# Kernel optimization log

Measured on AMD Instinct MI355X. Metric: run time of the kernel, lower is better.

## Reference

```python
import jax, jax.numpy as jnp
import numpy as np

B, L, W = 4096, 30, 5          # batch, MAX_TOKEN_LENGTH, WINDOW_SIZE
A, E = 30, 128                 # ALPHABET_SIZE, embedding dim
C = 40                         # OUT_CHANNELS
H, T = 128, 3                  # LSTM_UNITS, num CRF tags
LIN = W * C                    # 200
EPS = 1e-5


def setup_inputs():
    key = jax.random.key(0)
    ks = jax.random.split(key, 24)
    def rn(k, shape, s=0.1):
        return jax.random.normal(k, shape, jnp.float32) * s
    return {
        'x': jax.random.randint(ks[0], (B, L, W), 0, A, jnp.int32),
        'emb': rn(ks[1], (A, E), 1.0),
        'conv_w': rn(ks[2], (C, E, 3)),
        'conv_b': rn(ks[3], (C,)),
        'bn1_g': 1.0 + rn(ks[4], (C,)),
        'bn1_b': rn(ks[5], (C,)),
        'bn1_m': rn(ks[6], (C,)),
        'bn1_v': 0.5 + jax.random.uniform(ks[7], (C,), jnp.float32),
        'w_ih_f': rn(ks[8], (4 * H, LIN)),
        'w_hh_f': rn(ks[9], (4 * H, H)),
        'b_f': rn(ks[10], (4 * H,)),
        'w_ih_b': rn(ks[11], (4 * H, LIN)),
        'w_hh_b': rn(ks[12], (4 * H, H)),
        'b_b': rn(ks[13], (4 * H,)),
        'bn2_g': 1.0 + rn(ks[14], (2 * H,)),
        'bn2_b': rn(ks[15], (2 * H,)),
        'bn2_m': rn(ks[16], (2 * H,)),
        'bn2_v': 0.5 + jax.random.uniform(ks[17], (2 * H,), jnp.float32),
        'fc_w': rn(ks[18], (T, 2 * H)),
        'fc_b': rn(ks[19], (T,)),
        'trans': rn(ks[20], (T, T)),
        'start_t': rn(ks[21], (T,)),
        'end_t': rn(ks[22], (T,)),
    }


def _lstm_dir(seq, w_ih, w_hh, b, reverse):
    # seq: [B, L, F]; torch gate order i, f, g, o
    xs = jnp.einsum('blf,gf->lbg', seq, w_ih) + b  # [L, B, 4H]
    h0 = jnp.zeros((seq.shape[0], H), seq.dtype)
    def step(carry, xt):
        h, c = carry
        z = xt + h @ w_hh.T
        i, f, g, o = jnp.split(z, 4, axis=-1)
        c = jax.nn.sigmoid(f) * c + jax.nn.sigmoid(i) * jnp.tanh(g)
        h = jax.nn.sigmoid(o) * jnp.tanh(c)
        return (h, c), h
    _, hs = jax.lax.scan(step, (h0, h0), xs, reverse=reverse)
    return hs.transpose(1, 0, 2)  # [B, L, H]


def _viterbi(emis, mask, trans, start_t, end_t):
    # emis: [B, L, T], mask: [B, L] bool
    score = start_t + emis[:, 0]                      # [B, T]
    def step(score, inp):
        e_t, m_t = inp                                # [B, T], [B]
        cand = score[:, :, None] + trans              # [B, Tprev, Tnext]
        ptr = jnp.argmax(cand, axis=1)                # [B, T]
        new = jnp.max(cand, axis=1) + e_t
        return jnp.where(m_t[:, None], new, score), ptr
    score, hist = jax.lax.scan(
        step, score, (emis[:, 1:].transpose(1, 0, 2), mask[:, 1:].T))
    score = score + end_t
    best = jnp.max(score, axis=1)                     # [B] path scores
    last = jnp.argmax(score, axis=1)                  # [B]
    def back(tag, inp):
        h_t, m_t = inp
        prev = jnp.take_along_axis(h_t, tag[:, None], axis=1)[:, 0]
        tag = jnp.where(m_t, prev, tag)
        return tag, tag
    _, ys = jax.lax.scan(back, last, (hist, mask[:, 1:].T), reverse=True)
    tags = jnp.concatenate([ys, last[None]], axis=0).T  # [B, L]
    return best, tags


def reference(x, emb, conv_w, conv_b, bn1_g, bn1_b, bn1_m, bn1_v,
              w_ih_f, w_hh_f, b_f, w_ih_b, w_hh_b, b_b,
              bn2_g, bn2_b, bn2_m, bn2_v, fc_w, fc_b, trans, start_t, end_t):
    mask = x[:, :, 2] > 0                             # [B, L]
    e = emb[x.reshape(B * L, W)]                      # [N, W, E]  (dropout=eval noop)
    e = e.transpose(0, 2, 1)                          # [N, E, W]
    y = jax.lax.conv_general_dilated(
        e, conv_w, (1,), [(1, 1)],
        dimension_numbers=('NCH', 'OIH', 'NCH')) + conv_b[:, None]
    # BatchNorm1d (inference, running stats)
    y = (y - bn1_m[:, None]) * (bn1_g / jnp.sqrt(bn1_v + EPS))[:, None] + bn1_b[:, None]
    y = jax.nn.relu(y)
    # MaxPool1d(k=3, stride=1, pad=1): length preserved
    y = jax.lax.reduce_window(y, -jnp.inf, jax.lax.max,
                              (1, 1, 3), (1, 1, 1),
                              [(0, 0), (0, 0), (1, 1)])
    y = y.reshape(B, L, LIN)                          # torch.flatten is channel-major = row-major reshape
    hf = _lstm_dir(y, w_ih_f, w_hh_f, b_f, False)
    hb = _lstm_dir(y, w_ih_b, w_hh_b, b_b, True)
    h = jnp.concatenate([hf, hb], axis=-1)            # [B, L, 2H]
    h = (h - bn2_m) * (bn2_g / jnp.sqrt(bn2_v + EPS)) + bn2_b
    emis = h @ fc_w.T + fc_b                          # [B, L, T]
    return _viterbi(emis, mask, trans, start_t, end_t)
```

## Files before the change

kernel.cpp:

```cpp
#include <hip/hip_runtime.h>
#include <math.h>

#define BB    4096
#define LL    30
#define WW    5
#define CC    40
#define HH    128
#define TT    3
#define KA    328
#define NB    32
#define NT_   1024
#define FSTR  232
#define HSTR  136
#define CW    1056

#define WS_P    0
#define WS_BC   3600
#define WS_BG   3648
#define WS_WFC  4672
#define WS_EB   5440
#define WS_WBF  5504
#define WS_EMIS (5504 + 540672)

typedef __bf16 bf16x8 __attribute__((ext_vector_type(8)));
typedef float  f32x4  __attribute__((ext_vector_type(4)));
typedef unsigned short u16x8 __attribute__((ext_vector_type(8)));

__device__ __forceinline__ float sigm(float x) {
    return __builtin_amdgcn_rcpf(1.0f + __expf(-x));
}
__device__ __forceinline__ float tanh_fast(float x) {
    return 2.0f * __builtin_amdgcn_rcpf(1.0f + __expf(-2.0f * x)) - 1.0f;
}
__device__ __forceinline__ unsigned short f2bf(float f) {
    unsigned u = __builtin_bit_cast(unsigned, f);
    return (unsigned short)((u + 0x7FFFu + ((u >> 16) & 1u)) >> 16);
}
__device__ __forceinline__ float bf2f(unsigned short h) {
    unsigned u = ((unsigned)h) << 16;
    return __builtin_bit_cast(float, u);
}

__global__ void prep_kernel(const float* __restrict__ emb, const float* __restrict__ conv_w,
                            const float* __restrict__ conv_b,
                            const float* __restrict__ bn1_g, const float* __restrict__ bn1_b,
                            const float* __restrict__ bn1_m, const float* __restrict__ bn1_v,
                            const float* __restrict__ w_ih_f, const float* __restrict__ w_hh_f,
                            const float* __restrict__ b_f,
                            const float* __restrict__ w_ih_b, const float* __restrict__ w_hh_b,
                            const float* __restrict__ b_b,
                            const float* __restrict__ bn2_g, const float* __restrict__ bn2_b,
                            const float* __restrict__ bn2_m, const float* __restrict__ bn2_v,
                            const float* __restrict__ fc_w, const float* __restrict__ fc_b,
                            float* __restrict__ ws)
{
    const int gid = blockIdx.x * blockDim.x + threadIdx.x;
    const int gsz = gridDim.x * blockDim.x;

    for (int idx = gid; idx < 3600; idx += gsz) {
        int k = idx / 1200, rem = idx % 1200, a = rem / 40, c = rem % 40;
        float s1 = bn1_g[c] / sqrtf(bn1_v[c] + 1e-5f);
        float acc = 0.f;
        for (int e = 0; e < 128; ++e)
            acc += emb[a * 128 + e] * conv_w[(c * 128 + e) * 3 + k];
        ws[WS_P + idx] = acc * s1;
    }
    for (int c = gid; c < CC; c += gsz) {
        float s1 = bn1_g[c] / sqrtf(bn1_v[c] + 1e-5f);
        ws[WS_BC + c] = (conv_b[c] - bn1_m[c]) * s1 + bn1_b[c];
    }
    for (int i = gid; i < 1024; i += gsz) {
        int d = i >> 9, g = i & 511;
        ws[WS_BG + i] = d ? b_b[g] : b_f[g];
    }
    for (int i = gid; i < 768; i += gsz) {
        int d = i / 384, r = i % 384, t = r / 128, u = r % 128;
        int j = d * 128 + u;
        float s2 = bn2_g[j] / sqrtf(bn2_v[j] + 1e-5f);
        ws[WS_WFC + i] = fc_w[t * 256 + j] * s2;
    }
    for (int t = gid; t < TT; t += gsz) {
        float acc = fc_b[t];
        for (int j = 0; j < 256; ++j) {
            float s2 = bn2_g[j] / sqrtf(bn2_v[j] + 1e-5f);
            acc += fc_w[t * 256 + j] * (bn2_b[j] - bn2_m[j] * s2);
        }
        ws[WS_EB + t] = acc;
    }
    unsigned short* wsu = (unsigned short*)ws;
    for (int i = gid; i < 2 * 512 * CW; i += gsz) {
        int d = i / (512 * CW), r = i % (512 * CW);
        int n = r / CW, q = r % CW;
        int Ks = q / 96, t = q % 96, s = t / 32, k32 = t % 32;
        int k = Ks * 32 + k32;
        int u = n >> 2, g = n & 3, row = g * 128 + u;
        const float* wih = d ? w_ih_b : w_ih_f;
        const float* whh = d ? w_hh_b : w_hh_f;
        float w = (k < 200) ? wih[row * 200 + k]
                            : ((k >= 224) ? whh[row * 128 + (k - 224)] : 0.f);
        unsigned short t0 = f2bf(w);
        float r1 = w - bf2f(t0);
        unsigned short t1 = f2bf(r1);
        unsigned short t2 = f2bf(r1 - bf2f(t1));
        wsu[2 * WS_WBF + i] = (s == 0) ? t0 : ((s == 1) ? t1 : t2);
    }
}

__global__ __launch_bounds__(1024, 1)
void lstm_kernel(const int* __restrict__ x, float* __restrict__ ws)
{
    __shared__ unsigned short Fh[2][NB * FSTR], Fl[2][NB * FSTR], Fm[2][NB * FSTR];
    __shared__ unsigned short Hh[2][NB * HSTR], Hl[2][NB * HSTR], Hm[2][NB * HSTR];
    __shared__ float Pp_s[3600];
    __shared__ float Wfc_s[384];
    __shared__ float biasC_s[40];

    const int tid = threadIdx.x;
    const int d   = blockIdx.x & 1;
    const int b0  = (blockIdx.x >> 1) * NB;

    const unsigned short* __restrict__ Wb =
        (const unsigned short*)ws + 2 * WS_WBF + d * (512 * CW);
    float* emis = ws + WS_EMIS + d * (BB * LL * TT);

    for (int i = tid; i < 3600; i += NT_) Pp_s[i] = ws[WS_P + i];
    for (int i = tid; i < 384;  i += NT_) Wfc_s[i] = ws[WS_WFC + d * 384 + i];
    for (int i = tid; i < 40;   i += NT_) biasC_s[i] = ws[WS_BC + i];
    for (int i = tid; i < NB * FSTR; i += NT_) {
        ((unsigned*)Fh)[i] = 0u; ((unsigned*)Fl)[i] = 0u; ((unsigned*)Fm)[i] = 0u;
    }
    for (int i = tid; i < NB * HSTR; i += NT_) {
        ((unsigned*)Hh)[i] = 0u; ((unsigned*)Hl)[i] = 0u; ((unsigned*)Hm)[i] = 0u;
    }

    const int lane = tid & 63;
    const int wv   = tid >> 6;
    const int quad = lane >> 4;
    const int ml   = lane & 15;

    const unsigned short* __restrict__ Wn[2] = {
        Wb + (wv * 32 +  0 + ml) * CW + quad * 8,
        Wb + (wv * 32 + 16 + ml) * CW + quad * 8
    };

    const float* bgp = ws + WS_BG + d * 512;
    int   un[2];
    float bIv[2], bFv[2], bGv[2], bOv[2];
    #pragma unroll
    for (int nt = 0; nt < 2; ++nt) {
        int u = wv * 8 + nt * 4 + quad;
        un[nt]  = u;
        bIv[nt] = bgp[u];
        bFv[nt] = bgp[128 + u];
        bGv[nt] = bgp[256 + u];
        bOv[nt] = bgp[384 + u];
    }

    float cst[2][2];
    #pragma unroll
    for (int mt = 0; mt < 2; ++mt)
        #pragma unroll
        for (int nt = 0; nt < 2; ++nt) cst[mt][nt] = 0.f;

    __syncthreads();

#define FEAT_ONE(LPOS, BUF, P)                                                 \
    {                                                                          \
        int bb = (P) / CC, c = (P) % CC;                                       \
        const int* tok = x + (((b0 + bb) * LL) + (LPOS)) * WW;                 \
        int t0 = tok[0], t1 = tok[1], t2 = tok[2], t3 = tok[3], t4 = tok[4];   \
        float bc = biasC_s[c];                                                 \
        float a0 = bc + Pp_s[(30 + t0) * 40 + c] + Pp_s[(60 + t1) * 40 + c];   \
        float a1 = bc + Pp_s[t0 * 40 + c] + Pp_s[(30 + t1) * 40 + c] + Pp_s[(60 + t2) * 40 + c]; \
        float a2 = bc + Pp_s[t1 * 40 + c] + Pp_s[(30 + t2) * 40 + c] + Pp_s[(60 + t3) * 40 + c]; \
        float a3 = bc + Pp_s[t2 * 40 + c] + Pp_s[(30 + t3) * 40 + c] + Pp_s[(60 + t4) * 40 + c]; \
        float a4 = bc + Pp_s[t3 * 40 + c] + Pp_s[(30 + t4) * 40 + c];          \
        a0 = fmaxf(a0, 0.f); a1 = fmaxf(a1, 0.f); a2 = fmaxf(a2, 0.f);         \
        a3 = fmaxf(a3, 0.f); a4 = fmaxf(a4, 0.f);                              \
        float f[5];                                                            \
        f[0] = fmaxf(a0, a1);                                                  \
        f[1] = fmaxf(fmaxf(a0, a1), a2);                                       \
        f[2] = fmaxf(fmaxf(a1, a2), a3);                                       \
        f[3] = fmaxf(fmaxf(a2, a3), a4);                                       \
        f[4] = fmaxf(a3, a4);                                                  \
        int base = bb * FSTR + c * 5;                                          \
        _Pragma("unroll")                                                      \
        for (int j = 0; j < 5; ++j) {                                          \
            unsigned short h0 = f2bf(f[j]);                                    \
            float r1 = f[j] - bf2f(h0);                                        \
            unsigned short h1 = f2bf(r1);                                      \
            unsigned short h2 = f2bf(r1 - bf2f(h1));                           \
            Fh[BUF][base + j] = h0;                                            \
            Fl[BUF][base + j] = h1;                                            \
            Fm[BUF][base + j] = h2;                                            \
        }                                                                      \
    }

#define DO_FEATURES(LPOS, BUF)                                                 \
    FEAT_ONE(LPOS, BUF, tid)                                                   \
    if (tid >= 768) FEAT_ONE(LPOS, BUF, tid + 256)

    {
        const int l0 = d ? (LL - 1) : 0;
        DO_FEATURES(l0, 0)
    }
    __syncthreads();

    for (int step = 0; step < LL; ++step) {
        const int fb = step & 1;
        const int hw = step & 1;
        const int hr = hw ^ 1;

        f32x4 acc[2][2];
        #pragma unroll
        for (int mt = 0; mt < 2; ++mt)
            #pragma unroll
            for (int nt = 0; nt < 2; ++nt)
                acc[mt][nt] = (f32x4){0.f, 0.f, 0.f, 0.f};

#define WLOAD(B, P, KS)                                                        \
        {                                                                      \
            B[0] = *(const bf16x8*)((P) + (KS) * 96);                          \
            B[1] = *(const bf16x8*)((P) + (KS) * 96 + 32);                     \
            B[2] = *(const bf16x8*)((P) + (KS) * 96 + 64);                     \
        }
#define GEMM6(B, NT)                                                           \
        {                                                                      \
            acc[0][NT] = __builtin_amdgcn_mfma_f32_16x16x32_bf16(B[0], a0[0], acc[0][NT], 0, 0, 0); \
            acc[0][NT] = __builtin_amdgcn_mfma_f32_16x16x32_bf16(B[0], a0[1], acc[0][NT], 0, 0, 0); \
            acc[0][NT] = __builtin_amdgcn_mfma_f32_16x16x32_bf16(B[1], a0[0], acc[0][NT], 0, 0, 0); \
            acc[0][NT] = __builtin_amdgcn_mfma_f32_16x16x32_bf16(B[1], a0[1], acc[0][NT], 0, 0, 0); \
            acc[0][NT] = __builtin_amdgcn_mfma_f32_16x16x32_bf16(B[2], a0[0], acc[0][NT], 0, 0, 0); \
            acc[0][NT] = __builtin_amdgcn_mfma_f32_16x16x32_bf16(B[0], a0[2], acc[0][NT], 0, 0, 0); \
            acc[1][NT] = __builtin_amdgcn_mfma_f32_16x16x32_bf16(B[0], a1[0], acc[1][NT], 0, 0, 0); \
            acc[1][NT] = __builtin_amdgcn_mfma_f32_16x16x32_bf16(B[0], a1[1], acc[1][NT], 0, 0, 0); \
            acc[1][NT] = __builtin_amdgcn_mfma_f32_16x16x32_bf16(B[1], a1[0], acc[1][NT], 0, 0, 0); \
            acc[1][NT] = __builtin_amdgcn_mfma_f32_16x16x32_bf16(B[1], a1[1], acc[1][NT], 0, 0, 0); \
            acc[1][NT] = __builtin_amdgcn_mfma_f32_16x16x32_bf16(B[2], a1[0], acc[1][NT], 0, 0, 0); \
            acc[1][NT] = __builtin_amdgcn_mfma_f32_16x16x32_bf16(B[0], a1[2], acc[1][NT], 0, 0, 0); \
        }

        {
            bf16x8 wbuf[2][2][3];
            #pragma unroll
            for (int nt = 0; nt < 2; ++nt)
                WLOAD(wbuf[0][nt], Wn[nt], 0)

            #pragma unroll
            for (int Ks = 0; Ks < 11; ++Ks) {
                const int cur = Ks & 1, nxt = cur ^ 1;
                if (Ks < 10) {
                    #pragma unroll
                    for (int nt = 0; nt < 2; ++nt)
                        WLOAD(wbuf[nxt][nt], Wn[nt], Ks + 1)
                }
                bf16x8 a0[3], a1[3];
                if (Ks < 7) {
                    const int ko = Ks * 32 + quad * 8;
                    a0[0] = *(const bf16x8*)&Fh[fb][ml * FSTR + ko];
                    a0[1] = *(const bf16x8*)&Fl[fb][ml * FSTR + ko];
                    a0[2] = *(const bf16x8*)&Fm[fb][ml * FSTR + ko];
                    a1[0] = *(const bf16x8*)&Fh[fb][(16 + ml) * FSTR + ko];
                    a1[1] = *(const bf16x8*)&Fl[fb][(16 + ml) * FSTR + ko];
                    a1[2] = *(const bf16x8*)&Fm[fb][(16 + ml) * FSTR + ko];
                } else {
                    const int ko = (Ks - 7) * 32 + quad * 8;
                    a0[0] = *(const bf16x8*)&Hh[hr][ml * HSTR + ko];
                    a0[1] = *(const bf16x8*)&Hl[hr][ml * HSTR + ko];
                    a0[2] = *(const bf16x8*)&Hm[hr][ml * HSTR + ko];
                    a1[0] = *(const bf16x8*)&Hh[hr][(16 + ml) * HSTR + ko];
                    a1[1] = *(const bf16x8*)&Hl[hr][(16 + ml) * HSTR + ko];
                    a1[2] = *(const bf16x8*)&Hm[hr][(16 + ml) * HSTR + ko];
                }
                GEMM6(wbuf[cur][0], 0)
                GEMM6(wbuf[cur][1], 1)
            }
        }
#undef WLOAD
#undef GEMM6

        if (step + 1 < LL) {
            const int lnext = d ? (LL - 2 - step) : (step + 1);
            DO_FEATURES(lnext, (step + 1) & 1)
        }
        if (step > 0 && tid < 192) {
            const int lprev = d ? (LL - step) : (step - 1);
            int bb = tid / 6, r6 = tid % 6, t = r6 >> 1, seg = r6 & 1;
            int hoff = bb * HSTR + seg * 64;
            const float* wfc = &Wfc_s[t * 128 + seg * 64];
            float s = 0.f;
            #pragma unroll
            for (int i = 0; i < 8; ++i) {
                u16x8 v0 = *(const u16x8*)&Hh[hr][hoff + i * 8];
                u16x8 v1 = *(const u16x8*)&Hl[hr][hoff + i * 8];
                u16x8 v2 = *(const u16x8*)&Hm[hr][hoff + i * 8];
                #pragma unroll
                for (int j = 0; j < 8; ++j) {
                    float h = bf2f(v0[j]) + bf2f(v1[j]) + bf2f(v2[j]);
                    s += h * wfc[i * 8 + j];
                }
            }
            s += __shfl_xor(s, 1);
            if (seg == 0)
                emis[(((b0 + bb) * LL) + lprev) * TT + t] = s;
        }

        #pragma unroll
        for (int mt = 0; mt < 2; ++mt) {
            #pragma unroll
            for (int nt = 0; nt < 2; ++nt) {
                float zi = acc[mt][nt][0] + bIv[nt];
                float zf = acc[mt][nt][1] + bFv[nt];
                float zg = acc[mt][nt][2] + bGv[nt];
                float zo = acc[mt][nt][3] + bOv[nt];
                float cn = sigm(zf) * cst[mt][nt] + sigm(zi) * tanh_fast(zg);
                cst[mt][nt] = cn;
                float h = sigm(zo) * tanh_fast(cn);
                unsigned short h0 = f2bf(h);
                float r1 = h - bf2f(h0);
                unsigned short h1 = f2bf(r1);
                unsigned short h2 = f2bf(r1 - bf2f(h1));
                int idx = (mt * 16 + ml) * HSTR + un[nt];
                Hh[hw][idx] = h0;
                Hl[hw][idx] = h1;
                Hm[hw][idx] = h2;
            }
        }

        __syncthreads();
    }

    if (tid < 192) {
        const int llast = d ? 0 : (LL - 1);
        const int hl_ = (LL - 1) & 1;
        int bb = tid / 6, r6 = tid % 6, t = r6 >> 1, seg = r6 & 1;
        int hoff = bb * HSTR + seg * 64;
        const float* wfc = &Wfc_s[t * 128 + seg * 64];
        float s = 0.f;
        #pragma unroll
        for (int i = 0; i < 8; ++i) {
            u16x8 v0 = *(const u16x8*)&Hh[hl_][hoff + i * 8];
            u16x8 v1 = *(const u16x8*)&Hl[hl_][hoff + i * 8];
            u16x8 v2 = *(const u16x8*)&Hm[hl_][hoff + i * 8];
            #pragma unroll
            for (int j = 0; j < 8; ++j) {
                float h = bf2f(v0[j]) + bf2f(v1[j]) + bf2f(v2[j]);
                s += h * wfc[i * 8 + j];
            }
        }
        s += __shfl_xor(s, 1);
        if (seg == 0)
            emis[(((b0 + bb) * LL) + llast) * TT + t] = s;
    }
#undef DO_FEATURES
#undef FEAT_ONE
}

__global__ void viterbi_kernel(const int* __restrict__ x, const float* __restrict__ ws,
                               const float* __restrict__ trans,
                               const float* __restrict__ start_t,
                               const float* __restrict__ end_t,
                               float* __restrict__ out)
{
    int b = blockIdx.x * blockDim.x + threadIdx.x;
    if (b >= BB) return;
    const float* eF = ws + WS_EMIS;
    const float* eB = ws + WS_EMIS + BB * LL * TT;
    const float eb0 = ws[WS_EB + 0], eb1 = ws[WS_EB + 1], eb2 = ws[WS_EB + 2];
    float tr[9];
    #pragma unroll
    for (int i = 0; i < 9; ++i) tr[i] = trans[i];

    int base = b * LL * TT;
    float s0 = start_t[0] + eF[base + 0] + eB[base + 0] + eb0;
    float s1 = start_t[1] + eF[base + 1] + eB[base + 1] + eb1;
    float s2 = start_t[2] + eF[base + 2] + eB[base + 2] + eb2;

    unsigned hist[LL - 1];
    unsigned maskbits = 0;

    #pragma unroll
    for (int l = 1; l < LL; ++l) {
        bool m = x[(b * LL + l) * WW + 2] > 0;
        if (m) maskbits |= (1u << l);
        int idx = base + l * TT;
        float e0 = eF[idx + 0] + eB[idx + 0] + eb0;
        float e1 = eF[idx + 1] + eB[idx + 1] + eb1;
        float e2 = eF[idx + 2] + eB[idx + 2] + eb2;

        float ns[3]; int pt[3];
        #pragma unroll
        for (int nt = 0; nt < 3; ++nt) {
            float c0 = s0 + tr[0 * 3 + nt];
            float c1 = s1 + tr[1 * 3 + nt];
            float c2 = s2 + tr[2 * 3 + nt];
            int p = 0; float bc = c0;
            if (c1 > bc) { bc = c1; p = 1; }
            if (c2 > bc) { bc = c2; p = 2; }
            ns[nt] = bc; pt[nt] = p;
        }
        ns[0] += e0; ns[1] += e1; ns[2] += e2;
        hist[l - 1] = (unsigned)pt[0] | ((unsigned)pt[1] << 2) | ((unsigned)pt[2] << 4);
        if (m) { s0 = ns[0]; s1 = ns[1]; s2 = ns[2]; }
    }
    s0 += end_t[0]; s1 += end_t[1]; s2 += end_t[2];
    float best = s0; int last = 0;
    if (s1 > best) { best = s1; last = 1; }
    if (s2 > best) { best = s2; last = 2; }

    out[b] = best;
    float* tags = out + BB + b * LL;
    int tag = last;
    tags[LL - 1] = (float)last;
    #pragma unroll
    for (int l = LL - 1; l >= 1; --l) {
        int prev = (int)((hist[l - 1] >> (2 * tag)) & 3u);
        if (maskbits & (1u << l)) tag = prev;
        tags[l - 1] = (float)tag;
    }
}

extern "C" void kernel_launch(void* const* d_in, const int* in_sizes, int n_in,
                              void* d_out, int out_size, void* d_ws, size_t ws_size,
                              hipStream_t stream)
{
    const int*   x      = (const int*)  d_in[0];
    const float* emb    = (const float*)d_in[1];
    const float* conv_w = (const float*)d_in[2];
    const float* conv_b = (const float*)d_in[3];
    const float* bn1_g  = (const float*)d_in[4];
    const float* bn1_b  = (const float*)d_in[5];
    const float* bn1_m  = (const float*)d_in[6];
    const float* bn1_v  = (const float*)d_in[7];
    const float* w_ih_f = (const float*)d_in[8];
    const float* w_hh_f = (const float*)d_in[9];
    const float* b_f    = (const float*)d_in[10];
    const float* w_ih_b = (const float*)d_in[11];
    const float* w_hh_b = (const float*)d_in[12];
    const float* b_b    = (const float*)d_in[13];
    const float* bn2_g  = (const float*)d_in[14];
    const float* bn2_b  = (const float*)d_in[15];
    const float* bn2_m  = (const float*)d_in[16];
    const float* bn2_v  = (const float*)d_in[17];
    const float* fc_w   = (const float*)d_in[18];
    const float* fc_b   = (const float*)d_in[19];
    const float* trans  = (const float*)d_in[20];
    const float* start_t= (const float*)d_in[21];
    const float* end_t  = (const float*)d_in[22];

    float* ws  = (float*)d_ws;
    float* out = (float*)d_out;

    prep_kernel<<<256, 256, 0, stream>>>(emb, conv_w, conv_b,
                                         bn1_g, bn1_b, bn1_m, bn1_v,
                                         w_ih_f, w_hh_f, b_f,
                                         w_ih_b, w_hh_b, b_b,
                                         bn2_g, bn2_b, bn2_m, bn2_v,
                                         fc_w, fc_b, ws);
    lstm_kernel<<<256, 1024, 0, stream>>>(x, ws);
    viterbi_kernel<<<16, 256, 0, stream>>>(x, ws, trans, start_t, end_t, out);
}
```

Before: 747.9 us.

## Interleave feature and emission work into MFMA K-loop with staggered per-wave slots

Moves the next-step feature computation (conv/BN/pool splitting) and the previous-step emission dot products inside the recurrent GEMM K-loop. Each wave runs them at a different K-slice chosen by its wave index, so the scalar/LDS work can overlap with other waves' MFMA instead of running as a serial phase after the GEMM. It also hoists the first weight-tile prefetch out of the step loop and reissues it before the barrier for the next step. This adds code inside the unrolled loop and raises register pressure.

```diff
diff --git a/kernel.cpp b/kernel.cpp
--- a/kernel.cpp
+++ b/kernel.cpp
@@ -196,27 +196,33 @@
         }                                                                      \
     }
 
-#define DO_FEATURES(LPOS, BUF)                                                 \
-    FEAT_ONE(LPOS, BUF, tid)                                                   \
-    if (tid >= 768) FEAT_ONE(LPOS, BUF, tid + 256)
+#define EMIS_BODY(LPOS, HB)                                                    \
+    {                                                                          \
+        int bb = tid / 6, r6 = tid % 6, t = r6 >> 1, seg = r6 & 1;             \
+        int hoff = bb * HSTR + seg * 64;                                       \
+        const float* wfc = &Wfc_s[t * 128 + seg * 64];                         \
+        float s = 0.f;                                                         \
+        _Pragma("unroll")                                                      \
+        for (int i = 0; i < 8; ++i) {                                          \
+            u16x8 v0 = *(const u16x8*)&Hh[HB][hoff + i * 8];                   \
+            u16x8 v1 = *(const u16x8*)&Hl[HB][hoff + i * 8];                   \
+            u16x8 v2 = *(const u16x8*)&Hm[HB][hoff + i * 8];                   \
+            _Pragma("unroll")                                                  \
+            for (int j = 0; j < 8; ++j) {                                      \
+                float h = bf2f(v0[j]) + bf2f(v1[j]) + bf2f(v2[j]);             \
+                s += h * wfc[i * 8 + j];                                       \
+            }                                                                  \
+        }                                                                      \
+        s += __shfl_xor(s, 1);                                                 \
+        if (seg == 0)                                                          \
+            emis[(((b0 + bb) * LL) + (LPOS)) * TT + t] = s;                    \
+    }
 
     {
         const int l0 = d ? (LL - 1) : 0;
-        DO_FEATURES(l0, 0)
-    }
-    __syncthreads();
-
-    for (int step = 0; step < LL; ++step) {
-        const int fb = step & 1;
-        const int hw = step & 1;
-        const int hr = hw ^ 1;
-
-        f32x4 acc[2][2];
-        #pragma unroll
-        for (int mt = 0; mt < 2; ++mt)
-            #pragma unroll
-            for (int nt = 0; nt < 2; ++nt)
-                acc[mt][nt] = (f32x4){0.f, 0.f, 0.f, 0.f};
+        FEAT_ONE(l0, 0, tid)
+        if (tid >= 768) FEAT_ONE(l0, 0, tid + 256)
+    }
 
 #define WLOAD(B, P, KS)                                                        \
         {                                                                      \
@@ -240,12 +246,26 @@
             acc[1][NT] = __builtin_amdgcn_mfma_f32_16x16x32_bf16(B[0], a1[2], acc[1][NT], 0, 0, 0); \
         }
 
-        {
-            bf16x8 wbuf[2][2][3];
+    bf16x8 wbuf[2][2][3];
+    #pragma unroll
+    for (int nt = 0; nt < 2; ++nt)
+        WLOAD(wbuf[0][nt], Wn[nt], 0)
+
+    __syncthreads();
+
+    for (int step = 0; step < LL; ++step) {
+        const int fb = step & 1;
+        const int hw = step & 1;
+        const int hr = hw ^ 1;
+
+        f32x4 acc[2][2];
+        #pragma unroll
+        for (int mt = 0; mt < 2; ++mt)
             #pragma unroll
             for (int nt = 0; nt < 2; ++nt)
-                WLOAD(wbuf[0][nt], Wn[nt], 0)
-
+                acc[mt][nt] = (f32x4){0.f, 0.f, 0.f, 0.f};
+
+        {
             #pragma unroll
             for (int Ks = 0; Ks < 11; ++Ks) {
                 const int cur = Ks & 1, nxt = cur ^ 1;
@@ -274,35 +294,20 @@
                 }
                 GEMM6(wbuf[cur][0], 0)
                 GEMM6(wbuf[cur][1], 1)
-            }
-        }
-#undef WLOAD
-#undef GEMM6
-
-        if (step + 1 < LL) {
-            const int lnext = d ? (LL - 2 - step) : (step + 1);
-            DO_FEATURES(lnext, (step + 1) & 1)
-        }
-        if (step > 0 && tid < 192) {
-            const int lprev = d ? (LL - step) : (step - 1);
-            int bb = tid / 6, r6 = tid % 6, t = r6 >> 1, seg = r6 & 1;
-            int hoff = bb * HSTR + seg * 64;
-            const float* wfc = &Wfc_s[t * 128 + seg * 64];
-            float s = 0.f;
-            #pragma unroll
-            for (int i = 0; i < 8; ++i) {
-                u16x8 v0 = *(const u16x8*)&Hh[hr][hoff + i * 8];
-                u16x8 v1 = *(const u16x8*)&Hl[hr][hoff + i * 8];
-                u16x8 v2 = *(const u16x8*)&Hm[hr][hoff + i * 8];
-                #pragma unroll
-                for (int j = 0; j < 8; ++j) {
-                    float h = bf2f(v0[j]) + bf2f(v1[j]) + bf2f(v2[j]);
-                    s += h * wfc[i * 8 + j];
+
+                if (step + 1 < LL && Ks == (wv % 11)) {
+                    const int lnext = d ? (LL - 2 - step) : (step + 1);
+                    FEAT_ONE(lnext, fb ^ 1, tid)
+                }
+                if (step + 1 < LL && tid >= 768 && Ks == ((wv * 7 + 3) % 11)) {
+                    const int lnext = d ? (LL - 2 - step) : (step + 1);
+                    FEAT_ONE(lnext, fb ^ 1, tid + 256)
+                }
+                if (step > 0 && tid < 192 && Ks == 8 + wv) {
+                    const int lprev = d ? (LL - step) : (step - 1);
+                    EMIS_BODY(lprev, hr)
                 }
             }
-            s += __shfl_xor(s, 1);
-            if (seg == 0)
-                emis[(((b0 + bb) * LL) + lprev) * TT + t] = s;
         }
 
         #pragma unroll
@@ -327,32 +332,23 @@
             }
         }
 
+        if (step + 1 < LL) {
+            #pragma unroll
+            for (int nt = 0; nt < 2; ++nt)
+                WLOAD(wbuf[0][nt], Wn[nt], 0)
+        }
+
         __syncthreads();
     }
+#undef WLOAD
+#undef GEMM6
 
     if (tid < 192) {
         const int llast = d ? 0 : (LL - 1);
         const int hl_ = (LL - 1) & 1;
-        int bb = tid / 6, r6 = tid % 6, t = r6 >> 1, seg = r6 & 1;
-        int hoff = bb * HSTR + seg * 64;
-        const float* wfc = &Wfc_s[t * 128 + seg * 64];
-        float s = 0.f;
-        #pragma unroll
-        for (int i = 0; i < 8; ++i) {
-            u16x8 v0 = *(const u16x8*)&Hh[hl_][hoff + i * 8];
-            u16x8 v1 = *(const u16x8*)&Hl[hl_][hoff + i * 8];
-            u16x8 v2 = *(const u16x8*)&Hm[hl_][hoff + i * 8];
-            #pragma unroll
-            for (int j = 0; j < 8; ++j) {
-                float h = bf2f(v0[j]) + bf2f(v1[j]) + bf2f(v2[j]);
-                s += h * wfc[i * 8 + j];
-            }
-        }
-        s += __shfl_xor(s, 1);
-        if (seg == 0)
-            emis[(((b0 + bb) * LL) + llast) * TT + t] = s;
-    }
-#undef DO_FEATURES
+        EMIS_BODY(llast, hl_)
+    }
+#undef EMIS_BODY
 #undef FEAT_ONE
 }
 
```

Result: slower. 871.2 us (+16.5%).
